# Performance work log

Hardware: AMD Instinct MI355X
Metric: run time of the kernel (lower is better)

The kernel has to match this reference:

```python
import jax, jax.numpy as jnp
import numpy as np

H = 1024
NH = 16
HD = H // NH
EPS = 1e-5


def _layernorm(x, g, b):
    mu = jnp.mean(x, axis=-1, keepdims=True)
    var = jnp.mean((x - mu) ** 2, axis=-1, keepdims=True)
    return (x - mu) * jax.lax.rsqrt(var + EPS) * g + b


def setup_inputs() -> dict:
    key = jax.random.key(0)
    ks = jax.random.split(key, 12)
    s = lambda fan_in: 1.0 / np.sqrt(fan_in)
    x = jax.random.normal(ks[0], (2, 2048, H), dtype=jnp.float32)
    return {
        "x": x,
        "ln1_g": jnp.ones((H,), jnp.float32),
        "ln1_b": jnp.zeros((H,), jnp.float32),
        "W_qkv": jax.random.uniform(ks[1], (H, 3 * H), jnp.float32, -s(H), s(H)),
        "b_qkv": jax.random.uniform(ks[2], (3 * H,), jnp.float32, -s(H), s(H)),
        "W_out": jax.random.uniform(ks[3], (H, H), jnp.float32, -s(H), s(H)),
        "b_out": jax.random.uniform(ks[4], (H,), jnp.float32, -s(H), s(H)),
        "ln2_g": jnp.ones((H,), jnp.float32),
        "ln2_b": jnp.zeros((H,), jnp.float32),
        "W1": jax.random.uniform(ks[5], (H, 4 * H), jnp.float32, -s(H), s(H)),
        "b1": jax.random.uniform(ks[6], (4 * H,), jnp.float32, -s(H), s(H)),
        "W2": jax.random.uniform(ks[7], (4 * H, H), jnp.float32, -s(4 * H), s(4 * H)),
        "b2": jax.random.uniform(ks[8], (H,), jnp.float32, -s(4 * H), s(4 * H)),
    }


def reference(x, ln1_g, ln1_b, W_qkv, b_qkv, W_out, b_out, ln2_g, ln2_b, W1, b1, W2, b2):
    B, S, _ = x.shape
    residual = x
    h = _layernorm(x, ln1_g, ln1_b)
    qkv = h @ W_qkv + b_qkv                     # [B,S,3H]
    qkv = qkv.reshape(B, S, 3, NH, HD)
    q, k, v = qkv[:, :, 0], qkv[:, :, 1], qkv[:, :, 2]  # [B,S,NH,HD]
    scale = 1.0 / np.sqrt(HD)
    attn = jnp.einsum("bqhd,bkhd->bhqk", q, k) * scale  # [B,NH,S,S]
    attn = jax.nn.softmax(attn, axis=-1)
    out = jnp.einsum("bhqk,bkhd->bqhd", attn, v).reshape(B, S, H)
    x = residual + (out @ W_out + b_out)
    residual = x
    h = _layernorm(x, ln2_g, ln2_b)
    h = jax.nn.gelu(h @ W1 + b1, approximate=False) @ W2 + b2
    return residual + h
```

## Files before the change

### kernel.cpp

```cpp
#include <hip/hip_runtime.h>
#include <hip/hip_bf16.h>
#include <math.h>

#define HDIM 1024
#define SEQ  2048
#define BATCH 2
#define NHEAD 16
#define HEADD 64

typedef short bf16x8 __attribute__((ext_vector_type(8)));
typedef float f32x4  __attribute__((ext_vector_type(4)));
typedef unsigned short u16x8 __attribute__((ext_vector_type(8)));
typedef unsigned short u16x4 __attribute__((ext_vector_type(4)));

__device__ __forceinline__ unsigned short f2bf(float f) {
    unsigned u = __float_as_uint(f);
    unsigned r = (u + 0x7FFFu + ((u >> 16) & 1u)) >> 16;
    return (unsigned short)r;
}
__device__ __forceinline__ float b2f(unsigned short s) {
    return __uint_as_float(((unsigned)s) << 16);
}
__device__ __forceinline__ unsigned pk2bf(float lo, float hi) {
    __hip_bfloat162 h = __float22bfloat162_rn(float2{lo, hi});
    unsigned r;
    __builtin_memcpy(&r, &h, 4);
    return r;
}
__device__ __forceinline__ float fexp2(float x) {
#if __has_builtin(__builtin_amdgcn_exp2f)
    return __builtin_amdgcn_exp2f(x);
#else
    return exp2f(x);
#endif
}
__device__ __forceinline__ void gld16(void* lds, const void* g) {
    __builtin_amdgcn_global_load_lds(
        (const __attribute__((address_space(1))) unsigned int*)(g),
        (__attribute__((address_space(3))) unsigned int*)(lds),
        16, 0, 0);
}

#define SWZ(row, chunk) (((row) * 64) + (((chunk) ^ ((row) & 7)) << 3))

__device__ __forceinline__ void xcd_remap(int& bx, int& by) {
    int nx = gridDim.x, nwg = nx * gridDim.y;
    int hwid = by * nx + bx;
    int lid = (hwid & 7) * (nwg >> 3) + (hwid >> 3);
    bx = lid % nx;
    by = lid / nx;
}

__global__ __launch_bounds__(256) void ln_kernel(const float* __restrict__ x,
                                                 const float* __restrict__ gw,
                                                 const float* __restrict__ bw,
                                                 unsigned short* __restrict__ y)
{
    int row = blockIdx.x;
    int t = threadIdx.x;
    const float* xr = x + (size_t)row * HDIM;
    float4 v = *(const float4*)(xr + t * 4);
    float s1 = v.x + v.y + v.z + v.w;
    float s2 = v.x * v.x + v.y * v.y + v.z * v.z + v.w * v.w;
#pragma unroll
    for (int m = 1; m < 64; m <<= 1) {
        s1 += __shfl_xor(s1, m);
        s2 += __shfl_xor(s2, m);
    }
    __shared__ float red[8];
    int wid = t >> 6;
    if ((t & 63) == 0) { red[wid * 2] = s1; red[wid * 2 + 1] = s2; }
    __syncthreads();
    if (t == 0) {
        float a = red[0] + red[2] + red[4] + red[6];
        float b = red[1] + red[3] + red[5] + red[7];
        red[0] = a; red[1] = b;
    }
    __syncthreads();
    float mu  = red[0] * (1.0f / HDIM);
    float var = red[1] * (1.0f / HDIM) - mu * mu;
    float rs  = rsqrtf(var + 1e-5f);
    float4 g4 = *(const float4*)(gw + t * 4);
    float4 b4 = *(const float4*)(bw + t * 4);
    ushort4 o;
    o.x = f2bf((v.x - mu) * rs * g4.x + b4.x);
    o.y = f2bf((v.y - mu) * rs * g4.y + b4.y);
    o.z = f2bf((v.z - mu) * rs * g4.z + b4.z);
    o.w = f2bf((v.w - mu) * rs * g4.w + b4.w);
    *(ushort4*)(y + (size_t)row * HDIM + t * 4) = o;
}

__global__ __launch_bounds__(256) void wconv_all(const float* __restrict__ Wq,
                                                 const float* __restrict__ Wo,
                                                 const float* __restrict__ W1,
                                                 const float* __restrict__ W2,
                                                 unsigned short* __restrict__ WqT,
                                                 unsigned short* __restrict__ WoT,
                                                 unsigned short* __restrict__ W1T,
                                                 unsigned short* __restrict__ W2T)
{
    int bid = blockIdx.x;
    const float* W; unsigned short* WT; int K, nx, idx;
    if (bid < 3072)      { W = Wq; WT = WqT; K = 1024; nx = 96;  idx = bid; }
    else if (bid < 4096) { W = Wo; WT = WoT; K = 1024; nx = 32;  idx = bid - 3072; }
    else if (bid < 8192) { W = W1; WT = W1T; K = 1024; nx = 128; idx = bid - 4096; }
    else                 { W = W2; WT = W2T; K = 4096; nx = 32;  idx = bid - 8192; }
    int N = nx * 32;
    int n0 = (idx % nx) * 32, k0 = (idx / nx) * 32;

    __shared__ float tile[32][33];
    int t = threadIdx.x, c = t & 31, r = t >> 5;
#pragma unroll
    for (int i = 0; i < 4; ++i)
        tile[r + 8 * i][c] = W[(size_t)(k0 + r + 8 * i) * N + n0 + c];
    __syncthreads();
#pragma unroll
    for (int i = 0; i < 4; ++i)
        WT[(size_t)(n0 + r + 8 * i) * K + k0 + c] = f2bf(tile[c][r + 8 * i]);
}

template <int EPI>
__global__ __launch_bounds__(256, 2) void mgemm(const unsigned short* __restrict__ A,
                                                const unsigned short* __restrict__ BT,
                                                const float* __restrict__ bias,
                                                const float* __restrict__ resid,
                                                float* __restrict__ Cf,
                                                unsigned short* __restrict__ Cb,
                                                int M, int N, int K)
{
    __shared__ char smem[65536];
    int t = threadIdx.x;
    int bx = blockIdx.x, by = blockIdx.y;
    xcd_remap(bx, by);
    int bn = bx * 128, bm = by * 128;
    int l = t & 63, w = t >> 6;
    int wm = w >> 1, wn = w & 1;
    int lrow = l & 15, kq = l >> 4;

    f32x4 acc[4][4];
#pragma unroll
    for (int i = 0; i < 4; ++i)
#pragma unroll
        for (int j = 0; j < 4; ++j) acc[i][j] = {0.f, 0.f, 0.f, 0.f};

    const unsigned short* Ap[4];
    const unsigned short* Bp[4];
    int ld[4];
#pragma unroll
    for (int i = 0; i < 4; ++i) {
        int cid = i * 256 + t;
        int row = cid >> 3, c = cid & 7;
        int gc = (c ^ (row & 7)) << 3;
        Ap[i] = A + (size_t)(bm + row) * K + gc;
        Bp[i] = BT + (size_t)(bn + row) * K + gc;
        ld[i] = cid << 4;
    }

    int nt = K >> 6;
#pragma unroll
    for (int i = 0; i < 4; ++i) {
        gld16(smem + ld[i], Ap[i]);
        gld16(smem + 16384 + ld[i], Bp[i]);
    }
    __syncthreads();

    for (int tk = 0; tk < nt; ++tk) {
        int cur = (tk & 1) << 15;
        if (tk + 1 < nt) {
            int k0 = (tk + 1) << 6;
            int nxt = 32768 - cur;
#pragma unroll
            for (int i = 0; i < 4; ++i) {
                gld16(smem + nxt + ld[i], Ap[i] + k0);
                gld16(smem + nxt + 16384 + ld[i], Bp[i] + k0);
            }
        }
        const unsigned short* sA = (const unsigned short*)(smem + cur);
        const unsigned short* sB = (const unsigned short*)(smem + cur + 16384);
#pragma unroll
        for (int kk = 0; kk < 2; ++kk) {
            bf16x8 af[4], bv[4];
#pragma unroll
            for (int mi = 0; mi < 4; ++mi)
                af[mi] = *(const bf16x8*)(sA + SWZ(wm * 64 + mi * 16 + lrow, kk * 4 + kq));
#pragma unroll
            for (int ni = 0; ni < 4; ++ni)
                bv[ni] = *(const bf16x8*)(sB + SWZ(wn * 64 + ni * 16 + lrow, kk * 4 + kq));
#pragma unroll
            for (int mi = 0; mi < 4; ++mi)
#pragma unroll
                for (int ni = 0; ni < 4; ++ni)
                    acc[mi][ni] = __builtin_amdgcn_mfma_f32_16x16x32_bf16(af[mi], bv[ni], acc[mi][ni], 0, 0, 0);
        }
        __syncthreads();
    }

    int crow = (l >> 4) * 4;
    int ccol = l & 15;
#pragma unroll
    for (int mi = 0; mi < 4; ++mi) {
#pragma unroll
        for (int ni = 0; ni < 4; ++ni) {
            int gcol = bn + wn * 64 + ni * 16 + ccol;
            float bv = bias[gcol];
#pragma unroll
            for (int r = 0; r < 4; ++r) {
                int grow = bm + wm * 64 + mi * 16 + crow + r;
                size_t off = (size_t)grow * N + gcol;
                float v = acc[mi][ni][r] + bv;
                if (EPI == 1) {
                    Cf[off] = v + resid[off];
                } else if (EPI == 2) {
                    v = 0.5f * v * (1.0f + erff(v * 0.70710678118654752f));
                    Cb[off] = f2bf(v);
                } else {
                    Cb[off] = f2bf(v);
                }
            }
        }
    }
}

template <int EPI>
__global__ __launch_bounds__(256, 2) void mgemm64(const unsigned short* __restrict__ A,
                                                  const unsigned short* __restrict__ BT,
                                                  const float* __restrict__ bias,
                                                  const float* __restrict__ resid,
                                                  float* __restrict__ Cf,
                                                  unsigned short* __restrict__ Cb,
                                                  int M, int N, int K)
{
    __shared__ char smem[49152];
    int t = threadIdx.x;
    int bx = blockIdx.x, by = blockIdx.y;
    xcd_remap(bx, by);
    int bn = bx * 128, bm = by * 64;
    int l = t & 63, w = t >> 6;
    int lrow = l & 15, kq = l >> 4;

    f32x4 acc[4][2];
#pragma unroll
    for (int i = 0; i < 4; ++i)
#pragma unroll
        for (int j = 0; j < 2; ++j) acc[i][j] = {0.f, 0.f, 0.f, 0.f};

    const unsigned short* Ap[2];
    int ldA[2];
#pragma unroll
    for (int i = 0; i < 2; ++i) {
        int cid = i * 256 + t;
        int row = cid >> 3, c = cid & 7;
        Ap[i] = A + (size_t)(bm + row) * K + ((c ^ (row & 7)) << 3);
        ldA[i] = cid << 4;
    }
    const unsigned short* Bp[4];
    int ldB[4];
#pragma unroll
    for (int i = 0; i < 4; ++i) {
        int cid = i * 256 + t;
        int row = cid >> 3, c = cid & 7;
        Bp[i] = BT + (size_t)(bn + row) * K + ((c ^ (row & 7)) << 3);
        ldB[i] = cid << 4;
    }

    int nt = K >> 6;
#pragma unroll
    for (int i = 0; i < 2; ++i) gld16(smem + ldA[i], Ap[i]);
#pragma unroll
    for (int i = 0; i < 4; ++i) gld16(smem + 8192 + ldB[i], Bp[i]);
    __syncthreads();

    for (int tk = 0; tk < nt; ++tk) {
        int cur = (tk & 1) * 24576;
        if (tk + 1 < nt) {
            int k0 = (tk + 1) << 6;
            int nxt = 24576 - cur;
#pragma unroll
            for (int i = 0; i < 2; ++i) gld16(smem + nxt + ldA[i], Ap[i] + k0);
#pragma unroll
            for (int i = 0; i < 4; ++i) gld16(smem + nxt + 8192 + ldB[i], Bp[i] + k0);
        }
        const unsigned short* sA = (const unsigned short*)(smem + cur);
        const unsigned short* sB = (const unsigned short*)(smem + cur + 8192);
#pragma unroll
        for (int kk = 0; kk < 2; ++kk) {
            bf16x8 af[4], bv[2];
#pragma unroll
            for (int mi = 0; mi < 4; ++mi)
                af[mi] = *(const bf16x8*)(sA + SWZ(mi * 16 + lrow, kk * 4 + kq));
#pragma unroll
            for (int ni = 0; ni < 2; ++ni)
                bv[ni] = *(const bf16x8*)(sB + SWZ(w * 32 + ni * 16 + lrow, kk * 4 + kq));
#pragma unroll
            for (int mi = 0; mi < 4; ++mi)
#pragma unroll
                for (int ni = 0; ni < 2; ++ni)
                    acc[mi][ni] = __builtin_amdgcn_mfma_f32_16x16x32_bf16(af[mi], bv[ni], acc[mi][ni], 0, 0, 0);
        }
        __syncthreads();
    }

    int crow = (l >> 4) * 4;
    int ccol = l & 15;
#pragma unroll
    for (int mi = 0; mi < 4; ++mi) {
#pragma unroll
        for (int ni = 0; ni < 2; ++ni) {
            int gcol = bn + w * 32 + ni * 16 + ccol;
            float bv = bias[gcol];
#pragma unroll
            for (int r = 0; r < 4; ++r) {
                int grow = bm + mi * 16 + crow + r;
                size_t off = (size_t)grow * N + gcol;
                float v = acc[mi][ni][r] + bv;
                if (EPI == 1) {
                    Cf[off] = v + resid[off];
                } else if (EPI == 2) {
                    v = 0.5f * v * (1.0f + erff(v * 0.70710678118654752f));
                    Cb[off] = f2bf(v);
                } else {
                    Cb[off] = f2bf(v);
                }
            }
        }
    }
}

__global__ __launch_bounds__(512) void mattn(const unsigned short* __restrict__ qkv,
                                             unsigned short* __restrict__ out)
{
    __shared__ unsigned short Qs[128 * 64];
    __shared__ unsigned short Ks[2][64 * 64];
    __shared__ unsigned short Vt[2][64 * 64];
    __shared__ unsigned short Ps[8 * 16 * 64];
    int t = threadIdx.x;
    int w = t >> 6, l = t & 63;
    int lr = l & 15, lh = l >> 4;
    int q0 = blockIdx.x * 128;
    int hh = blockIdx.y, b = blockIdx.z;
    const unsigned short* Qg = qkv + (size_t)b * SEQ * 3072 + hh * 64;
    const unsigned short* Kg = Qg + 1024;
    const unsigned short* Vg = Qg + 2048;

#pragma unroll
    for (int i = 0; i < 2; ++i) {
        int chunkid = i * 512 + t;
        int row = chunkid >> 3, c = chunkid & 7;
        gld16(((char*)Qs) + chunkid * 16,
              Qg + (size_t)(q0 + row) * 3072 + ((c ^ (row & 7)) << 3));
    }

    int kr0 = t >> 3, kc0 = t & 7;
    const unsigned short* Kp0 = Kg + (size_t)kr0 * 3072 + kc0 * 8;
    int kd0 = SWZ(kr0, kc0);
    int vk = (t & 31) * 2;
    int vd0 = ((t >> 5) & 15) * 4;
    const unsigned short* Vp0 = Vg + (size_t)vk * 3072 + vd0;
    const unsigned short* Vp1 = Vp0 + 3072;

    u16x8 k0 = *(const u16x8*)Kp0;
    u16x4 v0 = *(const u16x4*)Vp0;
    u16x4 v1 = *(const u16x4*)Vp1;
    Kp0 += 64 * 3072; Vp0 += 64 * 3072; Vp1 += 64 * 3072;

    __syncthreads();
    bf16x8 qa[2];
#pragma unroll
    for (int ks = 0; ks < 2; ++ks)
        qa[ks] = *(const bf16x8*)(Qs + SWZ(w * 16 + lr, ks * 4 + lh));

    *(u16x8*)(Ks[0] + kd0) = k0;
#pragma unroll
    for (int j = 0; j < 4; ++j) {
        int d = vd0 + j;
        unsigned pack = (unsigned)(unsigned short)v0[j] | ((unsigned)(unsigned short)v1[j] << 16);
        *(unsigned*)(Vt[0] + SWZ(d, vk >> 3) + (vk & 7)) = pack;
    }
    k0 = *(const u16x8*)Kp0;
    v0 = *(const u16x4*)Vp0; v1 = *(const u16x4*)Vp1;
    Kp0 += 64 * 3072; Vp0 += 64 * 3072; Vp1 += 64 * 3072;
    asm volatile("s_waitcnt lgkmcnt(0)" ::: "memory");
    __builtin_amdgcn_s_barrier();

    f32x4 o[4];
#pragma unroll
    for (int i = 0; i < 4; ++i) o[i] = {0.f, 0.f, 0.f, 0.f};
    float mr = -3.0e38f, lsum = 0.f;
    unsigned short* Pw = Ps + w * (16 * 64);
    const float C = 0.18033688011112042f;

    const int nt = SEQ / 64;
    for (int tt = 0; tt < nt; ++tt) {
        const unsigned short* Kc = Ks[tt & 1];
        const unsigned short* Vc = Vt[tt & 1];

        f32x4 s[4];
#pragma unroll
        for (int ni = 0; ni < 4; ++ni) s[ni] = {0.f, 0.f, 0.f, 0.f};
#pragma unroll
        for (int ks = 0; ks < 2; ++ks) {
#pragma unroll
            for (int ni = 0; ni < 4; ++ni) {
                bf16x8 kb = *(const bf16x8*)(Kc + SWZ(ni * 16 + lr, ks * 4 + lh));
                s[ni] = __builtin_amdgcn_mfma_f32_16x16x32_bf16(kb, qa[ks], s[ni], 0, 0, 0);
            }
        }
        float mx = s[0][0];
#pragma unroll
        for (int ni = 0; ni < 4; ++ni)
#pragma unroll
            for (int r = 0; r < 4; ++r) mx = fmaxf(mx, s[ni][r]);
        mx = fmaxf(mx, __shfl_xor(mx, 16));
        mx = fmaxf(mx, __shfl_xor(mx, 32));
        if (__any(mx > mr + 64.0f)) {
            float mn = fmaxf(mr, mx);
            float corr = fexp2((mr - mn) * C);
            mr = mn;
            lsum *= corr;
            float cr[4];
#pragma unroll
            for (int r = 0; r < 4; ++r) cr[r] = __shfl(corr, lh * 4 + r, 16);
#pragma unroll
            for (int nd = 0; nd < 4; ++nd) {
                o[nd][0] *= cr[0]; o[nd][1] *= cr[1];
                o[nd][2] *= cr[2]; o[nd][3] *= cr[3];
            }
        }
        float mc = mr * C;
        float rsum = 0.f;
#pragma unroll
        for (int ni = 0; ni < 4; ++ni)
#pragma unroll
            for (int r = 0; r < 4; ++r) {
                float p = fexp2(fmaf(s[ni][r], C, -mc));
                s[ni][r] = p;
                rsum += p;
            }
        rsum += __shfl_xor(rsum, 16);
        rsum += __shfl_xor(rsum, 32);
        lsum += rsum;
#pragma unroll
        for (int ni = 0; ni < 4; ++ni)
#pragma unroll
            for (int rp = 0; rp < 2; ++rp) {
                int k = ni * 16 + lh * 4 + rp * 2;
                *(unsigned*)(Pw + SWZ(lr, k >> 3) + (k & 7)) =
                    pk2bf(s[ni][rp * 2], s[ni][rp * 2 + 1]);
            }
#pragma unroll
        for (int ks = 0; ks < 2; ++ks) {
            bf16x8 pa = *(const bf16x8*)(Pw + SWZ(lr, ks * 4 + lh));
#pragma unroll
            for (int nd = 0; nd < 4; ++nd) {
                bf16x8 vb = *(const bf16x8*)(Vc + SWZ(nd * 16 + lr, ks * 4 + lh));
                o[nd] = __builtin_amdgcn_mfma_f32_16x16x32_bf16(pa, vb, o[nd], 0, 0, 0);
            }
        }

        if (tt + 1 < nt) {
            int nb = (tt & 1) ^ 1;
            *(u16x8*)(Ks[nb] + kd0) = k0;
#pragma unroll
            for (int j = 0; j < 4; ++j) {
                int d = vd0 + j;
                unsigned pack = (unsigned)(unsigned short)v0[j] | ((unsigned)(unsigned short)v1[j] << 16);
                *(unsigned*)(Vt[nb] + SWZ(d, vk >> 3) + (vk & 7)) = pack;
            }
            if (tt + 2 < nt) {
                k0 = *(const u16x8*)Kp0;
                v0 = *(const u16x4*)Vp0; v1 = *(const u16x4*)Vp1;
                Kp0 += 64 * 3072; Vp0 += 64 * 3072; Vp1 += 64 * 3072;
            }
            asm volatile("s_waitcnt lgkmcnt(0)" ::: "memory");
            __builtin_amdgcn_s_barrier();
        }
    }
    float inv = 1.0f / lsum;
    float ir[4];
#pragma unroll
    for (int r = 0; r < 4; ++r) ir[r] = __shfl(inv, lh * 4 + r, 16);
#pragma unroll
    for (int r = 0; r < 4; ++r) {
        int q = q0 + w * 16 + lh * 4 + r;
#pragma unroll
        for (int nd = 0; nd < 4; ++nd) {
            int d = nd * 16 + lr;
            out[(size_t)((size_t)b * SEQ + q) * HDIM + hh * 64 + d] = f2bf(o[nd][r] * ir[r]);
        }
    }
}

extern "C" void kernel_launch(void* const* d_in, const int* in_sizes, int n_in,
                              void* d_out, int out_size, void* d_ws, size_t ws_size,
                              hipStream_t stream)
{
    const float* x     = (const float*)d_in[0];
    const float* ln1_g = (const float*)d_in[1];
    const float* ln1_b = (const float*)d_in[2];
    const float* W_qkv = (const float*)d_in[3];
    const float* b_qkv = (const float*)d_in[4];
    const float* W_out = (const float*)d_in[5];
    const float* b_out = (const float*)d_in[6];
    const float* ln2_g = (const float*)d_in[7];
    const float* ln2_b = (const float*)d_in[8];
    const float* W1    = (const float*)d_in[9];
    const float* b1    = (const float*)d_in[10];
    const float* W2    = (const float*)d_in[11];
    const float* b2    = (const float*)d_in[12];
    float* out = (float*)d_out;
    char* ws8  = (char*)d_ws;

    const int M = BATCH * SEQ;
    const size_t MB = 1048576;

    unsigned short* hbuf = (unsigned short*)(ws8);
    unsigned short* qkvb = (unsigned short*)(ws8 + 8 * MB);
    unsigned short* attb = (unsigned short*)(ws8 + 32 * MB);
    unsigned short* ffn1 = (unsigned short*)(ws8 + 8 * MB);
    unsigned short* WqT  = (unsigned short*)(ws8 + 40 * MB);
    unsigned short* WoT  = (unsigned short*)(ws8 + 46 * MB);
    unsigned short* W1T  = (unsigned short*)(ws8 + 48 * MB);
    unsigned short* W2T  = (unsigned short*)(ws8 + 56 * MB);

    wconv_all<<<12288, 256, 0, stream>>>(W_qkv, W_out, W1, W2, WqT, WoT, W1T, W2T);

    ln_kernel<<<M, 256, 0, stream>>>(x, ln1_g, ln1_b, hbuf);
    mgemm<0><<<dim3(3 * HDIM / 128, M / 128), 256, 0, stream>>>(hbuf, WqT, b_qkv, nullptr, nullptr, qkvb, M, 3 * HDIM, HDIM);
    mattn<<<dim3(SEQ / 128, NHEAD, BATCH), 512, 0, stream>>>(qkvb, attb);
    mgemm64<1><<<dim3(HDIM / 128, M / 64), 256, 0, stream>>>(attb, WoT, b_out, x, out, nullptr, M, HDIM, HDIM);
    ln_kernel<<<M, 256, 0, stream>>>(out, ln2_g, ln2_b, hbuf);
    mgemm<2><<<dim3(4 * HDIM / 128, M / 128), 256, 0, stream>>>(hbuf, W1T, b1, nullptr, nullptr, ffn1, M, 4 * HDIM, HDIM);
    mgemm64<1><<<dim3(HDIM / 128, M / 64), 256, 0, stream>>>(ffn1, W2T, b2, out, out, nullptr, M, HDIM, 4 * HDIM);
}
```

Before: 226.2 us.

## Permute B rows for vectorized GEMM epilogue stores, fast erf GELU, drop XCD remap

Permutes the rows of the B tile loaded into LDS so that each lane's MFMA output columns become contiguous. The epilogue can then do float4/float2 vector loads of bias and residual and vector stores of outputs instead of scalar strided accesses. It replaces erff in the GELU epilogue with an Abramowitz-Stegun polynomial using hardware rcp/exp2, trading a small accuracy loss for fewer instructions. It also removes the XCD block remapping, which may change L2 locality across chiplets.

Result: faster. 220.6 us (-2.5%).

```diff
diff --git a/kernel.cpp b/kernel.cpp
--- a/kernel.cpp
+++ b/kernel.cpp
@@ -17,9 +17,6 @@
     unsigned u = __float_as_uint(f);
     unsigned r = (u + 0x7FFFu + ((u >> 16) & 1u)) >> 16;
     return (unsigned short)r;
-}
-__device__ __forceinline__ float b2f(unsigned short s) {
-    return __uint_as_float(((unsigned)s) << 16);
 }
 __device__ __forceinline__ unsigned pk2bf(float lo, float hi) {
     __hip_bfloat162 h = __float22bfloat162_rn(float2{lo, hi});
@@ -34,6 +31,27 @@
     return exp2f(x);
 #endif
 }
+__device__ __forceinline__ float frcp(float x) {
+#if __has_builtin(__builtin_amdgcn_rcpf)
+    return __builtin_amdgcn_rcpf(x);
+#else
+    return 1.0f / x;
+#endif
+}
+__device__ __forceinline__ float erf_fast(float x) {
+    float ax = fabsf(x);
+    float t = frcp(fmaf(0.3275911f, ax, 1.0f));
+    float p = fmaf(t, 1.061405429f, -1.453152027f);
+    p = fmaf(p, t, 1.421413741f);
+    p = fmaf(p, t, -0.284496736f);
+    p = fmaf(p, t, 0.254829592f);
+    p *= t;
+    float e = fexp2(ax * ax * -1.4426950408889634f);
+    return copysignf(fmaf(-p, e, 1.0f), x);
+}
+__device__ __forceinline__ float gelu_f(float v) {
+    return 0.5f * v * (1.0f + erf_fast(v * 0.70710678118654752f));
+}
 __device__ __forceinline__ void gld16(void* lds, const void* g) {
     __builtin_amdgcn_global_load_lds(
         (const __attribute__((address_space(1))) unsigned int*)(g),
@@ -42,14 +60,6 @@
 }
 
 #define SWZ(row, chunk) (((row) * 64) + (((chunk) ^ ((row) & 7)) << 3))
-
-__device__ __forceinline__ void xcd_remap(int& bx, int& by) {
-    int nx = gridDim.x, nwg = nx * gridDim.y;
-    int hwid = by * nx + bx;
-    int lid = (hwid & 7) * (nwg >> 3) + (hwid >> 3);
-    bx = lid % nx;
-    by = lid / nx;
-}
 
 __global__ __launch_bounds__(256) void ln_kernel(const float* __restrict__ x,
                                                  const float* __restrict__ gw,
@@ -130,9 +140,7 @@
 {
     __shared__ char smem[65536];
     int t = threadIdx.x;
-    int bx = blockIdx.x, by = blockIdx.y;
-    xcd_remap(bx, by);
-    int bn = bx * 128, bm = by * 128;
+    int bn = blockIdx.x * 128, bm = blockIdx.y * 128;
     int l = t & 63, w = t >> 6;
     int wm = w >> 1, wn = w & 1;
     int lrow = l & 15, kq = l >> 4;
@@ -152,7 +160,8 @@
         int row = cid >> 3, c = cid & 7;
         int gc = (c ^ (row & 7)) << 3;
         Ap[i] = A + (size_t)(bm + row) * K + gc;
-        Bp[i] = BT + (size_t)(bn + row) * K + gc;
+        int prow = (row & 64) + ((row & 15) << 2) + ((row >> 4) & 3);
+        Bp[i] = BT + (size_t)(bn + prow) * K + gc;
         ld[i] = cid << 4;
     }
 
@@ -197,25 +206,28 @@
 
     int crow = (l >> 4) * 4;
     int ccol = l & 15;
+    int gcolb = bn + wn * 64 + ccol * 4;
+    float4 b4 = *(const float4*)(bias + gcolb);
 #pragma unroll
     for (int mi = 0; mi < 4; ++mi) {
 #pragma unroll
-        for (int ni = 0; ni < 4; ++ni) {
-            int gcol = bn + wn * 64 + ni * 16 + ccol;
-            float bv = bias[gcol];
-#pragma unroll
-            for (int r = 0; r < 4; ++r) {
-                int grow = bm + wm * 64 + mi * 16 + crow + r;
-                size_t off = (size_t)grow * N + gcol;
-                float v = acc[mi][ni][r] + bv;
-                if (EPI == 1) {
-                    Cf[off] = v + resid[off];
-                } else if (EPI == 2) {
-                    v = 0.5f * v * (1.0f + erff(v * 0.70710678118654752f));
-                    Cb[off] = f2bf(v);
-                } else {
-                    Cb[off] = f2bf(v);
+        for (int r = 0; r < 4; ++r) {
+            int grow = bm + wm * 64 + mi * 16 + crow + r;
+            size_t off = (size_t)grow * N + gcolb;
+            float v0 = acc[mi][0][r] + b4.x;
+            float v1 = acc[mi][1][r] + b4.y;
+            float v2 = acc[mi][2][r] + b4.z;
+            float v3 = acc[mi][3][r] + b4.w;
+            if (EPI == 1) {
+                float4 rr = *(const float4*)(resid + off);
+                float4 o4 = {v0 + rr.x, v1 + rr.y, v2 + rr.z, v3 + rr.w};
+                *(float4*)(Cf + off) = o4;
+            } else {
+                if (EPI == 2) {
+                    v0 = gelu_f(v0); v1 = gelu_f(v1); v2 = gelu_f(v2); v3 = gelu_f(v3);
                 }
+                ushort4 o4 = {f2bf(v0), f2bf(v1), f2bf(v2), f2bf(v3)};
+                *(ushort4*)(Cb + off) = o4;
             }
         }
     }
@@ -232,9 +244,7 @@
 {
     __shared__ char smem[49152];
     int t = threadIdx.x;
-    int bx = blockIdx.x, by = blockIdx.y;
-    xcd_remap(bx, by);
-    int bn = bx * 128, bm = by * 64;
+    int bn = blockIdx.x * 128, bm = blockIdx.y * 64;
     int l = t & 63, w = t >> 6;
     int lrow = l & 15, kq = l >> 4;
 
@@ -259,7 +269,8 @@
     for (int i = 0; i < 4; ++i) {
         int cid = i * 256 + t;
         int row = cid >> 3, c = cid & 7;
-        Bp[i] = BT + (size_t)(bn + row) * K + ((c ^ (row & 7)) << 3);
+        int prow = (row & ~31) + ((row & 15) << 1) + ((row >> 4) & 1);
+        Bp[i] = BT + (size_t)(bn + prow) * K + ((c ^ (row & 7)) << 3);
         ldB[i] = cid << 4;
     }
 
@@ -302,25 +313,23 @@
 
     int crow = (l >> 4) * 4;
     int ccol = l & 15;
+    int gcolb = bn + w * 32 + ccol * 2;
+    float2 b2 = *(const float2*)(bias + gcolb);
 #pragma unroll
     for (int mi = 0; mi < 4; ++mi) {
 #pragma unroll
-        for (int ni = 0; ni < 2; ++ni) {
-            int gcol = bn + w * 32 + ni * 16 + ccol;
-            float bv = bias[gcol];
-#pragma unroll
-            for (int r = 0; r < 4; ++r) {
-                int grow = bm + mi * 16 + crow + r;
-                size_t off = (size_t)grow * N + gcol;
-                float v = acc[mi][ni][r] + bv;
-                if (EPI == 1) {
-                    Cf[off] = v + resid[off];
-                } else if (EPI == 2) {
-                    v = 0.5f * v * (1.0f + erff(v * 0.70710678118654752f));
-                    Cb[off] = f2bf(v);
-                } else {
-                    Cb[off] = f2bf(v);
-                }
+        for (int r = 0; r < 4; ++r) {
+            int grow = bm + mi * 16 + crow + r;
+            size_t off = (size_t)grow * N + gcolb;
+            float v0 = acc[mi][0][r] + b2.x;
+            float v1 = acc[mi][1][r] + b2.y;
+            if (EPI == 1) {
+                float2 rr = *(const float2*)(resid + off);
+                float2 o2 = {v0 + rr.x, v1 + rr.y};
+                *(float2*)(Cf + off) = o2;
+            } else {
+                if (EPI == 2) { v0 = gelu_f(v0); v1 = gelu_f(v1); }
+                *(unsigned*)(Cb + off) = pk2bf(v0, v1);
             }
         }
     }
```
